# Optimization experiments

Measured on AMD Instinct MI355X. Metric: run time of the kernel, lower is better.

The kernel has to match this reference:

```python
import jax, jax.numpy as jnp
import numpy as np

B, C_IN, SEQ = 8, 512, 40
VOCAB, EMB = 30000, 300
NFILT = 256
KS = (2, 3, 4)
PATCH, IMG = 16, 384
NPR = IMG // PATCH          # 24 patches per row
NP_TOT = NPR * NPR          # 576 patches
MEAN = 0.5
STD = 0.5


def _conv_pool(x, w, b):
    # x: [N,1,SEQ,EMB], w: [NFILT,1,k,EMB] -> relu conv, max-pool over time -> [N,NFILT]
    y = jax.lax.conv_general_dilated(
        x, w, window_strides=(1, 1), padding='VALID',
        dimension_numbers=('NCHW', 'OIHW', 'NCHW'))  # [N,NFILT,SEQ-k+1,1]
    y = jax.nn.relu(y + b[None, :, None, None])
    return jnp.max(y[..., 0], axis=2)


def setup_inputs() -> dict:
    key = jax.random.key(0)
    ks = jax.random.split(key, 8)
    sentence_batch = jax.random.randint(ks[0], (B, C_IN, SEQ), 0, VOCAB, dtype=jnp.int64)
    W = jax.random.normal(ks[1], (VOCAB, EMB), dtype=jnp.float32)
    inp = {'sentence_batch': sentence_batch, 'W': W}
    for i, k in enumerate(KS):
        scale = 1.0 / np.sqrt(k * EMB)
        inp[f'conv_w{k}'] = jax.random.normal(ks[2 + 2 * i], (NFILT, 1, k, EMB), dtype=jnp.float32) * scale
        inp[f'conv_b{k}'] = jax.random.normal(ks[3 + 2 * i], (NFILT,), dtype=jnp.float32) * 0.01
    return inp


def reference(sentence_batch, W, conv_w2, conv_b2, conv_w3, conv_b3, conv_w4, conv_b4):
    convs = ((conv_w2, conv_b2), (conv_w3, conv_b3), (conv_w4, conv_b4))
    # textCNN (dropout is identity in eval mode)
    emb = W[sentence_batch]                              # [B,512,40,300]
    emb = emb.reshape(B * C_IN, 1, SEQ, EMB)             # [N,1,40,300]
    feats = jnp.concatenate([_conv_pool(emb, w, b) for w, b in convs], axis=1)  # [N,768]
    sent = feats.reshape(B, C_IN, 3, PATCH, PATCH)       # [B,512,3,16,16]
    # patch assembly: patch_idx >= L uses last patch (L-1)
    idx = jnp.minimum(jnp.arange(NP_TOT), C_IN - 1)      # [576]
    patches = sent[:, idx]                               # [B,576,3,16,16]
    img = patches.reshape(B, NPR, NPR, 3, PATCH, PATCH)
    img = img.transpose(0, 3, 1, 4, 2, 5).reshape(B, 3, IMG, IMG)
    pert_norm = jnp.linalg.norm(img.reshape(-1)) / B
    unnorm = img * STD + MEAN
    clipped = jnp.clip(unnorm, 0.0, 1.0)
    out = (clipped - MEAN) / STD
    return out, pert_norm
```

## Files before the change

### kernel.cpp

```cpp
#include <hip/hip_runtime.h>
#include <hip/hip_bf16.h>
#include <cstdint>

#define SEQ     40
#define EMB     300
#define NF      768
#define NKAPPA  40
#define IMGE    384
#define XROWS   51
#define XROWB   (XROWS * 640)
#define BLOB_OFF 256

using bf16x8 = short  __attribute__((ext_vector_type(8)));
using f32x4  = float  __attribute__((ext_vector_type(4)));

__device__ __forceinline__ unsigned short f2bf(float f) {
  unsigned int u = __builtin_bit_cast(unsigned int, f);
  u += 0x7FFFu + ((u >> 16) & 1u);
  return (unsigned short)(u >> 16);
}

__global__ __launch_bounds__(256) void prep_weights(
    const float* __restrict__ w2, const float* __restrict__ w3,
    const float* __restrict__ w4, unsigned short* __restrict__ blob)
{
  int kappa = blockIdx.x;
  int fq = blockIdx.y * 256 + threadIdx.x;
  int F = fq >> 2;
  int q = fq & 3;
  int j = kappa / 10, kk = kappa - 10 * j;
  int ch = F >> 8, f = F & 255;
  int k = ch + 2;
  const float* w = (ch == 0) ? w2 : (ch == 1 ? w3 : w4);

  bf16x8 pv;
  if (j < k) {
    const float* src = w + (size_t)(f * k + j) * 300;
    #pragma unroll
    for (int i = 0; i < 8; i++) {
      int e = kk * 32 + q * 8 + i;
      pv[i] = (e < 300) ? (short)f2bf(src[e]) : (short)0;
    }
  } else {
    #pragma unroll
    for (int i = 0; i < 8; i++) pv[i] = 0;
  }
  unsigned short* dst = blob + (size_t)(kappa * 768 + F) * 32 + q * 8;
  *(bf16x8*)dst = pv;
}

__global__ __launch_bounds__(512, 2) void main_conv(
    const int*  __restrict__ sb,   const float* __restrict__ W,
    const float* __restrict__ b2,  const float* __restrict__ b3,
    const float* __restrict__ b4,  const unsigned short* __restrict__ blob,
    float* __restrict__ out, float* __restrict__ nrm)
{
  __shared__ __align__(128) char X[2 * XROWB];
  const int tid = threadIdx.x;
  const int wv  = tid >> 6;
  const int l   = tid & 63;
  const int l15 = l & 15;
  const int hi  = l >> 4;
  const int sp  = blockIdx.x;

  for (int off = tid * 16; off < 2 * XROWB; off += 512 * 16)
    *(f32x4*)(X + off) = f32x4{0.f, 0.f, 0.f, 0.f};
  __syncthreads();

  for (int idx = tid; idx < 6000; idx += 512) {
    int s   = idx / 3000;
    int rem = idx - s * 3000;
    int r   = rem / 75;
    int c4  = rem - r * 75;
    int Sid = sp * 2 + s;
    int tok = sb[Sid * 40 + r];
    float4 wvv = *(const float4*)(W + (size_t)tok * 300 + c4 * 4);
    uint2 pk;
    pk.x = (unsigned)f2bf(wvv.x) | ((unsigned)f2bf(wvv.y) << 16);
    pk.y = (unsigned)f2bf(wvv.z) | ((unsigned)f2bf(wvv.w) << 16);
    int colbyte = c4 * 8;
    int off = s * XROWB + r * 640 + (colbyte ^ ((r & 7) << 4));
    *(uint2*)(X + off) = pk;
  }
  __syncthreads();

  f32x4 acc[2][3][6];
  #pragma unroll
  for (int s = 0; s < 2; s++)
    #pragma unroll
    for (int m = 0; m < 3; m++)
      #pragma unroll
      for (int n = 0; n < 6; n++)
        acc[s][m][n] = f32x4{0.f, 0.f, 0.f, 0.f};

  const char* bb = (const char*)blob + (size_t)(wv * 96 + l15) * 64 + hi * 16;

  #pragma unroll
  for (int j = 0; j < 4; j++) {
    for (int kk = 0; kk < 10; kk++) {
      int kappa = j * 10 + kk;
      bf16x8 Bf[6];
      #pragma unroll
      for (int n = 0; n < 6; n++)
        Bf[n] = *(const bf16x8*)(bb + (size_t)kappa * 49152 + n * 1024);
      #pragma unroll
      for (int s = 0; s < 2; s++) {
        bf16x8 Af[3];
        #pragma unroll
        for (int m = 0; m < 3; m++) {
          int row = 16 * m + l15 + j;
          int colbyte = kk * 64 + hi * 16;
          int off = s * XROWB + row * 640 + (colbyte ^ ((row & 7) << 4));
          Af[m] = *(const bf16x8*)(X + off);
        }
        #pragma unroll
        for (int m = 0; m < 3; m++)
          #pragma unroll
          for (int n = 0; n < 6; n++)
            acc[s][m][n] = __builtin_amdgcn_mfma_f32_16x16x32_bf16(
                Af[m], Bf[n], acc[s][m][n], 0, 0, 0);
      }
    }
  }

  float ss = 0.f;
  #pragma unroll
  for (int s = 0; s < 2; s++) {
    int Sid = sp * 2 + s;
    int b = Sid >> 9, c = Sid & 511;
    #pragma unroll
    for (int n = 0; n < 6; n++) {
      int F  = wv * 96 + n * 16 + l15;
      int ch = F >> 8;
      int plim = 39 - ch;
      float vmax = -1e30f;
      #pragma unroll
      for (int m = 0; m < 3; m++) {
        #pragma unroll
        for (int rg = 0; rg < 4; rg++) {
          int p = 16 * m + 4 * hi + rg;
          if (p < plim) vmax = fmaxf(vmax, acc[s][m][n][rg]);
        }
      }
      vmax = fmaxf(vmax, __shfl_xor(vmax, 16, 64));
      vmax = fmaxf(vmax, __shfl_xor(vmax, 32, 64));
      const float* bias = (ch == 0) ? b2 : (ch == 1 ? b3 : b4);
      float val = fmaxf(vmax + bias[F & 255], 0.f);
      if (hi == 0) {
        float mult = (c == 511) ? 65.f : 1.f;
        ss += mult * val * val;
        float st = fminf(val, 1.f);
        int fi = F & 255;
        int pi = fi >> 4, pj = fi & 15;
        if (c < 511) {
          int pr = c / 24, pc = c - pr * 24;
          out[((size_t)(b * 3 + ch) * IMGE + pr * 16 + pi) * IMGE + pc * 16 + pj] = st;
        } else {
          for (int pidx = 511; pidx < 576; pidx++) {
            int pr = pidx / 24, pc = pidx - pr * 24;
            out[((size_t)(b * 3 + ch) * IMGE + pr * 16 + pi) * IMGE + pc * 16 + pj] = st;
          }
        }
      }
    }
  }
  #pragma unroll
  for (int off = 32; off; off >>= 1) ss += __shfl_xor(ss, off, 64);
  if (l == 0) atomicAdd(nrm, ss);
}

__global__ void finalize(const float* __restrict__ nrm, float* __restrict__ out) {
  if (threadIdx.x == 0) out[3538944] = sqrtf(nrm[0]) * 0.125f;
}

extern "C" void kernel_launch(void* const* d_in, const int* in_sizes, int n_in,
                              void* d_out, int out_size, void* d_ws, size_t ws_size,
                              hipStream_t stream)
{
  const int*   sb = (const int*)d_in[0];
  const float* W  = (const float*)d_in[1];
  const float* w2 = (const float*)d_in[2];
  const float* b2 = (const float*)d_in[3];
  const float* w3 = (const float*)d_in[4];
  const float* b3 = (const float*)d_in[5];
  const float* w4 = (const float*)d_in[6];
  const float* b4 = (const float*)d_in[7];
  float* out = (float*)d_out;
  float* nrm = (float*)d_ws;
  unsigned short* blob = (unsigned short*)((char*)d_ws + BLOB_OFF);

  hipMemsetAsync(d_ws, 0, 8, stream);
  prep_weights<<<dim3(40, 12), 256, 0, stream>>>(w2, w3, w4, blob);
  main_conv<<<2048, 512, 0, stream>>>(sb, W, b2, b3, b4, blob, out, nrm);
  finalize<<<1, 64, 0, stream>>>(nrm, out);
}
```

Measured before the change: 511.6 us.

## Remap filters per wave to skip zero-padded taps and prefetch B fragments

Each wave now takes two 16-filter groups from every conv size (k=2,3,4) instead of a contiguous range of 96 filters. Because of this, the MFMAs for taps j that exceed a size's kernel length can be skipped uniformly for all waves (j=2 skips k=2, j=3 skips k=2,3). This removes the multiplications by zero-padded weights. B fragments for the next kk step are also loaded one iteration ahead to hide global latency, and A fragments are loaded for both sentences up front. The cost is more live registers, which could pressure occupancy at launch bounds (512,2).

```diff
diff --git a/kernel.cpp b/kernel.cpp
--- a/kernel.cpp
+++ b/kernel.cpp
@@ -4,8 +4,6 @@
 
 #define SEQ     40
 #define EMB     300
-#define NF      768
-#define NKAPPA  40
 #define IMGE    384
 #define XROWS   51
 #define XROWB   (XROWS * 640)
@@ -93,33 +91,49 @@
       for (int n = 0; n < 6; n++)
         acc[s][m][n] = f32x4{0.f, 0.f, 0.f, 0.f};
 
-  const char* bb = (const char*)blob + (size_t)(wv * 96 + l15) * 64 + hi * 16;
+  const char* bb = (const char*)blob + (size_t)l15 * 64 + hi * 16;
+  int Foff[6];
+  #pragma unroll
+  for (int n = 0; n < 6; n++)
+    Foff[n] = ((n >> 1) * 256 + (wv * 2 + (n & 1)) * 16) * 64;
 
   #pragma unroll
   for (int j = 0; j < 4; j++) {
+    const int nmin = (j < 2) ? 0 : (j - 1) * 2;
+    bf16x8 Bf[6];
+    #pragma unroll
+    for (int n = 0; n < 6; n++)
+      if (n >= nmin)
+        Bf[n] = *(const bf16x8*)(bb + (size_t)(j * 10) * 49152 + Foff[n]);
     for (int kk = 0; kk < 10; kk++) {
-      int kappa = j * 10 + kk;
-      bf16x8 Bf[6];
+      int kapn = j * 10 + (kk < 9 ? kk + 1 : 9);
+      bf16x8 Bn[6];
       #pragma unroll
       for (int n = 0; n < 6; n++)
-        Bf[n] = *(const bf16x8*)(bb + (size_t)kappa * 49152 + n * 1024);
-      #pragma unroll
-      for (int s = 0; s < 2; s++) {
-        bf16x8 Af[3];
+        if (n >= nmin)
+          Bn[n] = *(const bf16x8*)(bb + (size_t)kapn * 49152 + Foff[n]);
+      bf16x8 Af[2][3];
+      int colbyte = kk * 64 + hi * 16;
+      #pragma unroll
+      for (int s = 0; s < 2; s++)
         #pragma unroll
         for (int m = 0; m < 3; m++) {
           int row = 16 * m + l15 + j;
-          int colbyte = kk * 64 + hi * 16;
           int off = s * XROWB + row * 640 + (colbyte ^ ((row & 7) << 4));
-          Af[m] = *(const bf16x8*)(X + off);
+          Af[s][m] = *(const bf16x8*)(X + off);
         }
+      #pragma unroll
+      for (int s = 0; s < 2; s++)
         #pragma unroll
         for (int m = 0; m < 3; m++)
           #pragma unroll
           for (int n = 0; n < 6; n++)
-            acc[s][m][n] = __builtin_amdgcn_mfma_f32_16x16x32_bf16(
-                Af[m], Bf[n], acc[s][m][n], 0, 0, 0);
-      }
+            if (n >= nmin)
+              acc[s][m][n] = __builtin_amdgcn_mfma_f32_16x16x32_bf16(
+                  Af[s][m], Bf[n], acc[s][m][n], 0, 0, 0);
+      #pragma unroll
+      for (int n = 0; n < 6; n++)
+        if (n >= nmin) Bf[n] = Bn[n];
     }
   }
 
@@ -130,8 +144,8 @@
     int b = Sid >> 9, c = Sid & 511;
     #pragma unroll
     for (int n = 0; n < 6; n++) {
-      int F  = wv * 96 + n * 16 + l15;
-      int ch = F >> 8;
+      int ch = n >> 1;
+      int F  = ch * 256 + (wv * 2 + (n & 1)) * 16 + l15;
       int plim = 39 - ch;
       float vmax = -1e30f;
       #pragma unroll
```

After: 454.0 us. -11.3%, faster.
